# Optimization experiments

Hardware: AMD Instinct MI355X
Metric: run time of the kernel (lower is better)

## Reference

```python
import math
import jax, jax.numpy as jnp
import numpy as np

D_K = 1024


def setup_inputs() -> dict:
    key = jax.random.key(0)
    ks = jax.random.split(key, 7)
    B, L, d_model, d_k = 8, 2048, 1024, D_K
    source = jax.random.normal(ks[0], (B, L, d_model), dtype=jnp.float32)
    # torch nn.Linear params: weight (out, in), bias (out,)
    Wq = jax.random.normal(ks[1], (d_k, d_model), dtype=jnp.float32) * 0.02
    Wk = jax.random.normal(ks[2], (d_k, d_model), dtype=jnp.float32) * 0.02
    Wv = jax.random.normal(ks[3], (d_k, d_model), dtype=jnp.float32) * 0.02
    bq = jnp.zeros((d_k,), dtype=jnp.float32)
    bk = jnp.zeros((d_k,), dtype=jnp.float32)
    bv = jnp.zeros((d_k,), dtype=jnp.float32)
    return {"source": source, "Wq": Wq, "bq": bq, "Wk": Wk, "bk": bk,
            "Wv": Wv, "bv": bv, "mask": 1}


def reference(source, Wq, bq, Wk, bk, Wv, bv, mask):
    # q,k,v: (B, L, d_k); torch Linear => x @ W.T + b
    q = jnp.einsum("bld,kd->blk", source, Wq) + bq
    k = jnp.einsum("bld,kd->blk", source, Wk) + bk
    v = jnp.einsum("bld,kd->blk", source, Wv) + bv  # target defaults to source
    L = source.shape[1]
    scores = jnp.einsum("blk,bmk->blm", q, k) / math.sqrt(D_K)  # (B, L, L)
    if mask:
        # -inf strictly above the diagonal (j > i)
        causal = jnp.triu(jnp.full((L, L), -jnp.inf, dtype=scores.dtype), k=1)
        scores = scores + causal
    # Faithful to original: Softmax(dim=1) -> normalize over axis 1 (rows)
    attention = jax.nn.softmax(scores, axis=1)
    output = jnp.einsum("blm,bmk->blk", attention, v)  # (B, L, d_k)
    return (output, attention)
```

## Files before the change

kernel.cpp:

```cpp
#include <hip/hip_runtime.h>
#include <hip/hip_bf16.h>

typedef __attribute__((ext_vector_type(8))) __bf16 bf16x8;
typedef __attribute__((ext_vector_type(8))) unsigned short us8;
typedef __attribute__((ext_vector_type(4))) float f32x4;
typedef long long ll;

#define GLD(gp, lp) __builtin_amdgcn_global_load_lds( \
    (const __attribute__((address_space(1))) void*)(gp), \
    (__attribute__((address_space(3))) void*)(lp), 16, 0, 0)

#define SBAR()  asm volatile("s_barrier" ::: "memory")
#define VMCNT4  asm volatile("s_waitcnt vmcnt(4)" ::: "memory")
#define VMCNT0  asm volatile("s_waitcnt vmcnt(0)" ::: "memory")
#define SCHED0() __builtin_amdgcn_sched_barrier(0)

template<int OP>
__global__ __launch_bounds__(512) void gemm8(
    const __bf16* __restrict__ A, const __bf16* __restrict__ B,
    void* __restrict__ Cp, const float* __restrict__ bias,
    const int* __restrict__ maskp, float* __restrict__ part,
    int K, int lda, int ldb, int ldc,
    ll batchA, ll batchB, ll batchC)
{
    __shared__ __bf16 LA[2][256][64];
    __shared__ __bf16 LB[2][256][64];

    const int bx = blockIdx.x, by = blockIdx.y, bz = blockIdx.z;
    const int t    = threadIdx.x;
    const int w    = t >> 6, lane = t & 63;
    const int wrm  = w >> 2, wcn  = w & 3;
    const int fr   = lane & 15, fq = lane >> 4;
    const int row0 = bx * 256;
    const int col0 = by * 256;
    const int msk  = (OP >= 1) ? maskp[0] : 0;

    if (OP == 1 && msk && by > bx) {
        __bf16* C = (__bf16*)Cp + (ll)bz * batchC;
        bf16x8 z = {};
        #pragma unroll 4
        for (int pass = 0; pass < 16; ++pass) {
            int r = pass * 16 + (t >> 5);
            *(bf16x8*)&C[(ll)(row0 + r) * ldc + col0 + (t & 31) * 8] = z;
        }
        if (part && t < 256) part[((ll)bx * 8 + bz) * 2048 + col0 + t] = 0.f;
        return;
    }

    int NT = K / 64;
    if (OP == 2 && msk) NT = (row0 + 256) / 64;
    const int NI = NT / 2;

    const __bf16* Ab = A + (ll)bz * batchA;
    const __bf16* Bb = B + (ll)bz * batchB;

    const int srow = lane >> 3;
    const int cg   = (lane & 7) ^ srow;

    auto stageA = [&](int kt, int h, int slot) {
        #pragma unroll
        for (int is = 0; is < 2; ++is)
            GLD(Ab + (ll)(row0 + h*128 + is*64 + w*8 + srow) * lda + kt*64 + cg*8,
                &LA[slot][h*128 + is*64 + w*8][0]);
    };
    auto stageB = [&](int kt, int h, int slot) {
        #pragma unroll
        for (int is = 0; is < 2; ++is)
            GLD(Bb + (ll)(col0 + h*128 + is*64 + w*8 + srow) * ldb + kt*64 + cg*8,
                &LB[slot][h*128 + is*64 + w*8][0]);
    };
    auto rdA = [&](int slot, int row, int g) -> bf16x8 {
        return *(const bf16x8*)&LA[slot][row][(g ^ (row & 7)) << 3];
    };
    auto rdB = [&](int slot, int row, int g) -> bf16x8 {
        return *(const bf16x8*)&LB[slot][row][(g ^ (row & 7)) << 3];
    };

    f32x4  acc[8][4] = {};
    bf16x8 bB[4][2];

    stageA(0, 0, 0); stageA(0, 1, 0);
    stageB(0, 0, 0); stageB(0, 1, 0);
    stageB(1, 0, 1); stageB(1, 1, 1);
    VMCNT4;
    SBAR();

#define PHASE(SLOT, Q, STG, VMC) \
  { \
    if (Q == 0) { \
      _Pragma("unroll") for (int j = 0; j < 4; ++j) \
      _Pragma("unroll") for (int ks = 0; ks < 2; ++ks) \
        bB[j][ks] = rdB(SLOT, wcn*64 + j*16 + fr, ks*4 + fq); \
    } \
    bf16x8 bA[2][2]; \
    _Pragma("unroll") for (int fi = 0; fi < 2; ++fi) \
    _Pragma("unroll") for (int ks = 0; ks < 2; ++ks) \
      bA[fi][ks] = rdA(SLOT, wrm*128 + (Q*2+fi)*16 + fr, ks*4 + fq); \
    STG; \
    VMC; \
    SBAR(); SCHED0(); \
    __builtin_amdgcn_s_setprio(1); \
    _Pragma("unroll") for (int fi = 0; fi < 2; ++fi) \
    _Pragma("unroll") for (int j = 0; j < 4; ++j) \
    _Pragma("unroll") for (int ks = 0; ks < 2; ++ks) \
      acc[Q*2+fi][j] = __builtin_amdgcn_mfma_f32_16x16x32_bf16( \
          bA[fi][ks], bB[j][ks], acc[Q*2+fi][j], 0, 0, 0); \
    __builtin_amdgcn_s_setprio(0); \
    SCHED0(); SBAR(); \
  }

    for (int i = 0; i < NI; ++i) {
        const bool nl = (i < NI - 1);
        const int k1 = 2*i + 1, k2 = 2*i + 2, k3 = 2*i + 3;
        PHASE(0, 0, stageA(k1, 0, 1), );
        PHASE(0, 1, stageA(k1, 1, 1), );
        PHASE(0, 2, if (nl) stageB(k2, 0, 0), );
        PHASE(0, 3, if (nl) stageB(k2, 1, 0), if (nl) { VMCNT4; } else { VMCNT0; });
        PHASE(1, 0, if (nl) stageA(k2, 0, 0), );
        PHASE(1, 1, if (nl) stageA(k2, 1, 0), );
        PHASE(1, 2, if (nl) stageB(k3, 0, 1), );
        PHASE(1, 3, if (nl) stageB(k3, 1, 1), if (nl) { VMCNT4; });
    }
#undef PHASE

    const ll coff = (ll)bz * batchC;
    float s4[4] = {0.f, 0.f, 0.f, 0.f};
    #pragma unroll
    for (int fi = 0; fi < 8; ++fi)
    #pragma unroll
    for (int j = 0; j < 4; ++j)
    #pragma unroll
    for (int r4 = 0; r4 < 4; ++r4) {
        const int row = row0 + wrm*128 + fi*16 + fq*4 + r4;
        const int col = col0 + wcn*64 + j*16 + fr;
        float v = acc[fi][j][r4];
        if (OP == 0) {
            v += bias[col];
            ((__bf16*)Cp)[coff + (ll)row * ldc + col] = (__bf16)v;
        } else if (OP == 1) {
            float e = (msk && col > row) ? 0.f : __expf(v * 0.03125f);
            __bf16 eb = (__bf16)e;
            ((__bf16*)Cp)[coff + (ll)row * ldc + col] = eb;
            s4[j] += (float)eb;
        } else {
            ((float*)Cp)[coff + (ll)row * ldc + col] = v;
        }
    }
    if (OP == 1 && part != nullptr) {
        float* red = (float*)&LA[0][0][0];
        __syncthreads();
        #pragma unroll
        for (int j = 0; j < 4; ++j)
            red[(wrm*4 + fq)*256 + wcn*64 + j*16 + fr] = s4[j];
        __syncthreads();
        if (t < 256) {
            float tot = 0.f;
            #pragma unroll
            for (int r = 0; r < 8; ++r) tot += red[r*256 + t];
            part[((ll)bx * 8 + bz) * 2048 + col0 + t] = tot;
        }
    }
}

__global__ __launch_bounds__(512) void pv64(
    const __bf16* __restrict__ E, const __bf16* __restrict__ VT,
    const float* __restrict__ inv, float* __restrict__ out,
    float* __restrict__ attn, const int* __restrict__ maskp)
{
    __shared__ __bf16 LA[2][64][64];
    __shared__ __bf16 LB[2][256][64];

    const int bxr = (int)gridDim.x - 1 - (int)blockIdx.x;
    const int by = blockIdx.y, bz = blockIdx.z;
    const int t = threadIdx.x, w = t >> 6, lane = t & 63;
    const int wrm = w >> 2, wcn = w & 3;
    const int fr = lane & 15, fq = lane >> 4;
    const int row0 = bxr * 64, col0 = by * 256;
    const int msk = maskp[0];

    int NT = msk ? ((bxr + 2) & ~1) : 32;
    const int NI = NT / 2;

    const __bf16* Ab = E  + (ll)bz * 2048 * 2048;
    const __bf16* Bb = VT + (ll)bz * 1024 * 2048;

    const int srow = lane >> 3;
    const int cg   = (lane & 7) ^ srow;

    auto stageA = [&](int kt, int slot) {
        GLD(Ab + (ll)(row0 + w*8 + srow) * 2048 + kt*64 + cg*8,
            &LA[slot][w*8][0]);
    };
    auto stageB = [&](int kt, int slot) {
        #pragma unroll
        for (int h = 0; h < 2; ++h)
        #pragma unroll
        for (int is = 0; is < 2; ++is)
            GLD(Bb + (ll)(col0 + h*128 + is*64 + w*8 + srow) * 2048 + kt*64 + cg*8,
                &LB[slot][h*128 + is*64 + w*8][0]);
    };
    auto rdA = [&](int slot, int row, int g) -> bf16x8 {
        return *(const bf16x8*)&LA[slot][row][(g ^ (row & 7)) << 3];
    };
    auto rdB = [&](int slot, int row, int g) -> bf16x8 {
        return *(const bf16x8*)&LB[slot][row][(g ^ (row & 7)) << 3];
    };

    f32x4  acc[2][4] = {};
    bf16x8 bB[4][2];

    stageA(0, 0); stageB(0, 0);
    stageB(1, 1);
    VMCNT4;
    SBAR();

#define PHASEP(SLOT, Q, STG, VMC) \
  { \
    if (Q == 0) { \
      _Pragma("unroll") for (int j = 0; j < 4; ++j) \
      _Pragma("unroll") for (int ks = 0; ks < 2; ++ks) \
        bB[j][ks] = rdB(SLOT, wcn*64 + j*16 + fr, ks*4 + fq); \
    } \
    bf16x8 bA[2]; \
    _Pragma("unroll") for (int ks = 0; ks < 2; ++ks) \
      bA[ks] = rdA(SLOT, wrm*32 + Q*16 + fr, ks*4 + fq); \
    STG; \
    VMC; \
    SBAR(); SCHED0(); \
    __builtin_amdgcn_s_setprio(1); \
    _Pragma("unroll") for (int j = 0; j < 4; ++j) \
    _Pragma("unroll") for (int ks = 0; ks < 2; ++ks) \
      acc[Q][j] = __builtin_amdgcn_mfma_f32_16x16x32_bf16( \
          bA[ks], bB[j][ks], acc[Q][j], 0, 0, 0); \
    __builtin_amdgcn_s_setprio(0); \
    SCHED0(); SBAR(); \
  }

    for (int i = 0; i < NI; ++i) {
        const bool nl = (i < NI - 1);
        const int kb = 2*i + 1, ka2 = 2*i + 2, kb2 = 2*i + 3;
        PHASEP(0, 0, stageA(kb, 1), );
        PHASEP(0, 1, if (nl) stageB(ka2, 0),
                     if (nl) { VMCNT4; } else { VMCNT0; });
        PHASEP(1, 0, if (nl) stageA(ka2, 0), );
        PHASEP(1, 1, if (nl) stageB(kb2, 1),
                     if (nl) { VMCNT4; });
    }
#undef PHASEP

    #pragma unroll
    for (int qf = 0; qf < 2; ++qf)
    #pragma unroll
    for (int j = 0; j < 4; ++j)
    #pragma unroll
    for (int r4 = 0; r4 < 4; ++r4) {
        const int row = row0 + wrm*32 + qf*16 + fq*4 + r4;
        const int col = col0 + wcn*64 + j*16 + fr;
        out[(ll)bz*2048*1024 + (ll)row*1024 + col] = acc[qf][j][r4];
    }

    {
        const int c0 = by * 512;
        const int ct = (t & 63) * 8;
        float iv[8];
        #pragma unroll
        for (int e = 0; e < 8; ++e) iv[e] = inv[bz*2048 + c0 + ct + e];
        const int r00 = t >> 6;
        #pragma unroll 2
        for (int ri = 0; ri < 8; ++ri) {
            const int row = row0 + ri*8 + r00;
            bf16x8 ev = *(const bf16x8*)&Ab[(ll)row*2048 + c0 + ct];
            f32x4 lo, hi;
            #pragma unroll
            for (int e = 0; e < 4; ++e) {
                lo[e] = (float)ev[e]     * iv[e];
                hi[e] = (float)ev[e + 4] * iv[e + 4];
            }
            float* ao = attn + (ll)bz*2048*2048 + (ll)row*2048 + c0 + ct;
            ((f32x4*)ao)[0] = lo;
            ((f32x4*)ao)[1] = hi;
        }
    }
}

__global__ __launch_bounds__(256) void cvt_k(const float* __restrict__ in,
                                             __bf16* __restrict__ out, int n8)
{
    const int i = blockIdx.x * 256 + threadIdx.x;
    if (i >= n8) return;
    const f32x4* p = (const f32x4*)(in + (ll)i * 8);
    f32x4 a = p[0], b = p[1];
    bf16x8 h;
    #pragma unroll
    for (int j = 0; j < 4; ++j) { h[j] = (__bf16)a[j]; h[j + 4] = (__bf16)b[j]; }
    *(bf16x8*)(out + (ll)i * 8) = h;
}

__global__ __launch_bounds__(256) void cvtb_k(const float* __restrict__ q,
                                              const float* __restrict__ k,
                                              const float* __restrict__ v,
                                              float* __restrict__ bb)
{
    const int i = blockIdx.x * 256 + threadIdx.x;
    bb[i] = (i < 1024) ? q[i] : (i < 2048) ? k[i - 1024] : v[i - 2048];
}

__global__ __launch_bounds__(256) void rsum_k(const float* __restrict__ part,
                                              float* __restrict__ inv)
{
    const int idx = blockIdx.x * 256 + threadIdx.x;
    const int b = idx >> 11, m = idx & 2047;
    float s = 0.f;
    #pragma unroll
    for (int lc = 0; lc < 8; ++lc) s += part[((ll)lc * 8 + b) * 2048 + m];
    inv[idx] = 1.0f / s;
}

__global__ __launch_bounds__(256) void vtp_k(const __bf16* __restrict__ qkv,
                                             const float* __restrict__ inv,
                                             __bf16* __restrict__ vt)
{
    __shared__ __bf16 tile[64][72];
    const int t  = threadIdx.x;
    const int m0 = blockIdx.x * 64;
    const int k0 = blockIdx.y * 64;
    const int b  = blockIdx.z;

    const __bf16* V = qkv + (ll)b * 2048 * 3072 + 2048;
    #pragma unroll
    for (int h = 0; h < 2; ++h) {
        int r = (t >> 3) + h * 32;
        int c = (t & 7) * 8;
        int m = m0 + r;
        const float iv = inv[b * 2048 + m];
        bf16x8 v = *(const bf16x8*)&V[(ll)m * 3072 + k0 + c];
        bf16x8 o;
        #pragma unroll
        for (int j = 0; j < 8; ++j) o[j] = (__bf16)((float)v[j] * iv);
        *(bf16x8*)&tile[r][c] = o;
    }
    __syncthreads();
    __bf16* O = vt + (ll)b * 1024 * 2048;
    #pragma unroll
    for (int h = 0; h < 2; ++h) {
        int k = (t >> 3) + h * 32;
        int m = (t & 7) * 8;
        bf16x8 o;
        #pragma unroll
        for (int j = 0; j < 8; ++j) o[j] = tile[m + j][k];
        *(bf16x8*)&O[(ll)(k0 + k) * 2048 + m0 + m] = o;
    }
}

__global__ __launch_bounds__(256) void vt_k(const unsigned short* __restrict__ qkv,
                                            unsigned short* __restrict__ vt)
{
    __shared__ unsigned short tile[64][72];
    const int t  = threadIdx.x;
    const int m0 = blockIdx.x * 64;
    const int k0 = blockIdx.y * 64;
    const int b  = blockIdx.z;

    const unsigned short* V = qkv + (ll)b * 2048 * 3072 + 2048;
    #pragma unroll
    for (int h = 0; h < 2; ++h) {
        int r = (t >> 3) + h * 32;
        int c = (t & 7) * 8;
        us8 v = *(const us8*)&V[(ll)(m0 + r) * 3072 + k0 + c];
        *(us8*)&tile[r][c] = v;
    }
    __syncthreads();
    unsigned short* O = vt + (ll)b * 1024 * 2048;
    #pragma unroll
    for (int h = 0; h < 2; ++h) {
        int k = (t >> 3) + h * 32;
        int m = (t & 7) * 8;
        us8 o;
        #pragma unroll
        for (int j = 0; j < 8; ++j) o[j] = tile[m + j][k];
        *(us8*)&O[(ll)(k0 + k) * 2048 + m0 + m] = o;
    }
}

__global__ __launch_bounds__(256) void colsum_k(const __bf16* __restrict__ E,
                                                float* __restrict__ part)
{
    const int lc = blockIdx.x, mc = blockIdx.y, b = blockIdx.z;
    const int m  = mc * 256 + threadIdx.x;
    const __bf16* p = E + (ll)b * 2048 * 2048 + (ll)(lc * 256) * 2048 + m;
    float s = 0.f;
    #pragma unroll 4
    for (int l = 0; l < 256; ++l) s += (float)p[(ll)l * 2048];
    part[((ll)lc * 8 + b) * 2048 + m] = s;
}

__global__ __launch_bounds__(256) void norm_k(const __bf16* __restrict__ E,
                                              const float* __restrict__ part,
                                              float* __restrict__ attn,
                                              __bf16* __restrict__ attn_bf)
{
    const int lc = blockIdx.x, mc = blockIdx.y, b = blockIdx.z;
    const int m  = mc * 256 + threadIdx.x;
    float s = 0.f;
    #pragma unroll
    for (int j = 0; j < 8; ++j) s += part[((ll)j * 8 + b) * 2048 + m];
    const float iv = 1.0f / s;
    const __bf16* p = E + (ll)b * 2048 * 2048 + (ll)(lc * 256) * 2048 + m;
    float*  qo = attn    + (ll)b * 2048 * 2048 + (ll)(lc * 256) * 2048 + m;
    __bf16* ro = attn_bf + (ll)b * 2048 * 2048 + (ll)(lc * 256) * 2048 + m;
    #pragma unroll 4
    for (int l = 0; l < 256; ++l) {
        float a = (float)p[(ll)l * 2048] * iv;
        qo[(ll)l * 2048] = a;
        ro[(ll)l * 2048] = (__bf16)a;
    }
}

extern "C" void kernel_launch(void* const* d_in, const int* in_sizes, int n_in,
                              void* d_out, int out_size, void* d_ws, size_t ws_size,
                              hipStream_t stream)
{
    const float* X   = (const float*)d_in[0];
    const float* Wq  = (const float*)d_in[1];
    const float* bq  = (const float*)d_in[2];
    const float* Wk  = (const float*)d_in[3];
    const float* bk  = (const float*)d_in[4];
    const float* Wv  = (const float*)d_in[5];
    const float* bv  = (const float*)d_in[6];
    const int*   msk = (const int*)d_in[7];

    float* out  = (float*)d_out;
    float* attn = out + (ll)8 * 2048 * 1024;

    __bf16* Xb = (__bf16*)attn;
    __bf16* Wb = Xb + (ll)16384 * 1024;
    float*  bb = (float*)(Wb + (ll)3072 * 1024);

    __bf16* qkv = (__bf16*)d_ws;
    __bf16* vt  = qkv + (ll)16384 * 3072;

    cvt_k<<<dim3(8192), 256, 0, stream>>>(X, Xb, 16384 * 1024 / 8);
    cvt_k<<<dim3(512),  256, 0, stream>>>(Wq, Wb,               1024 * 1024 / 8);
    cvt_k<<<dim3(512),  256, 0, stream>>>(Wk, Wb + 1024 * 1024, 1024 * 1024 / 8);
    cvt_k<<<dim3(512),  256, 0, stream>>>(Wv, Wb + 2048 * 1024, 1024 * 1024 / 8);
    cvtb_k<<<dim3(12),  256, 0, stream>>>(bq, bk, bv, bb);

    gemm8<0><<<dim3(64, 12, 1), 512, 0, stream>>>(
        Xb, Wb, qkv, bb, msk, nullptr,
        1024, 1024, 1024, 3072, 0LL, 0LL, 0LL);

    const size_t need_fused =
        (size_t)(16384ll*3072 + 8ll*1024*2048 + 8ll*2048*2048) * 2
        + (size_t)(8*8*2048 + 8*2048) * 4;

    if (ws_size >= need_fused) {
        __bf16* E   = vt + (ll)8 * 1024 * 2048;
        float*  prt = (float*)(E + (ll)8 * 2048 * 2048);
        float*  inv = prt + 8 * 8 * 2048;

        gemm8<1><<<dim3(8, 8, 8), 512, 0, stream>>>(
            qkv, qkv + 1024, E, nullptr, msk, prt,
            1024, 3072, 3072, 2048,
            (ll)2048 * 3072, (ll)2048 * 3072, (ll)2048 * 2048);

        rsum_k<<<dim3(64), 256, 0, stream>>>(prt, inv);

        vtp_k<<<dim3(32, 16, 8), 256, 0, stream>>>(qkv, inv, vt);

        pv64<<<dim3(32, 4, 8), 512, 0, stream>>>(E, vt, inv, out, attn, msk);
    } else {
        __bf16* E   = (__bf16*)d_out;
        float*  prt = (float*)(vt + (ll)8 * 1024 * 2048);
        __bf16* attn_bf = qkv;

        vt_k<<<dim3(32, 16, 8), 256, 0, stream>>>((const unsigned short*)qkv,
                                                  (unsigned short*)vt);

        gemm8<1><<<dim3(8, 8, 8), 512, 0, stream>>>(
            qkv, qkv + 1024, E, nullptr, msk, nullptr,
            1024, 3072, 3072, 2048,
            (ll)2048 * 3072, (ll)2048 * 3072, (ll)2048 * 2048);

        colsum_k<<<dim3(8, 8, 8), 256, 0, stream>>>(E, prt);
        norm_k<<<dim3(8, 8, 8), 256, 0, stream>>>(E, prt, attn, attn_bf);

        gemm8<2><<<dim3(8, 4, 8), 512, 0, stream>>>(
            attn_bf, vt, out, nullptr, msk, nullptr,
            2048, 2048, 2048, 1024,
            (ll)2048 * 2048, (ll)1024 * 2048, (ll)2048 * 1024);
    }
}
```

Before: 336.7 us.

## Split attention normalization out of PV kernel and reorder PV block mapping

Moves the attention-probability write (E scaled by column inverse sums, widened to fp32) out of the PV GEMM epilogue into a separate norm2m_k kernel. That kernel zero-fills the masked upper tiles directly without reading E. The PV grid is flattened so the four column blocks of a row tile run next to each other, aiming for better reuse of the E row tile in cache. The cost is an extra launch and a separate pass over E, and the new kernel uses 4-byte per-thread strided row accesses that may coalesce less well than the old 8-wide vector stores.

```diff
diff --git a/kernel.cpp b/kernel.cpp
--- a/kernel.cpp
+++ b/kernel.cpp
@@ -164,14 +164,15 @@
 
 __global__ __launch_bounds__(512) void pv64(
     const __bf16* __restrict__ E, const __bf16* __restrict__ VT,
-    const float* __restrict__ inv, float* __restrict__ out,
-    float* __restrict__ attn, const int* __restrict__ maskp)
+    float* __restrict__ out, const int* __restrict__ maskp)
 {
     __shared__ __bf16 LA[2][64][64];
     __shared__ __bf16 LB[2][256][64];
 
-    const int bxr = (int)gridDim.x - 1 - (int)blockIdx.x;
-    const int by = blockIdx.y, bz = blockIdx.z;
+    const int n   = blockIdx.x;
+    const int by  = n & 3;
+    const int bxr = 31 - (n >> 2);
+    const int bz  = blockIdx.z;
     const int t = threadIdx.x, w = t >> 6, lane = t & 63;
     const int wrm = w >> 2, wcn = w & 3;
     const int fr = lane & 15, fq = lane >> 4;
@@ -258,29 +259,28 @@
         const int col = col0 + wcn*64 + j*16 + fr;
         out[(ll)bz*2048*1024 + (ll)row*1024 + col] = acc[qf][j][r4];
     }
-
-    {
-        const int c0 = by * 512;
-        const int ct = (t & 63) * 8;
-        float iv[8];
-        #pragma unroll
-        for (int e = 0; e < 8; ++e) iv[e] = inv[bz*2048 + c0 + ct + e];
-        const int r00 = t >> 6;
-        #pragma unroll 2
-        for (int ri = 0; ri < 8; ++ri) {
-            const int row = row0 + ri*8 + r00;
-            bf16x8 ev = *(const bf16x8*)&Ab[(ll)row*2048 + c0 + ct];
-            f32x4 lo, hi;
-            #pragma unroll
-            for (int e = 0; e < 4; ++e) {
-                lo[e] = (float)ev[e]     * iv[e];
-                hi[e] = (float)ev[e + 4] * iv[e + 4];
-            }
-            float* ao = attn + (ll)bz*2048*2048 + (ll)row*2048 + c0 + ct;
-            ((f32x4*)ao)[0] = lo;
-            ((f32x4*)ao)[1] = hi;
-        }
-    }
+}
+
+__global__ __launch_bounds__(256) void norm2m_k(const __bf16* __restrict__ E,
+                                                const float* __restrict__ inv,
+                                                float* __restrict__ attn,
+                                                const int* __restrict__ maskp)
+{
+    const int lc = blockIdx.x, mc = blockIdx.y, b = blockIdx.z;
+    const int m  = mc * 256 + threadIdx.x;
+    float* qo = attn + (ll)b * 2048 * 2048 + (ll)(lc * 256) * 2048 + m;
+
+    if (maskp[0] && mc > lc) {
+        #pragma unroll 4
+        for (int l = 0; l < 256; ++l)
+            qo[(ll)l * 2048] = 0.f;
+        return;
+    }
+    const float iv = inv[b * 2048 + m];
+    const __bf16* p = E + (ll)b * 2048 * 2048 + (ll)(lc * 256) * 2048 + m;
+    #pragma unroll 4
+    for (int l = 0; l < 256; ++l)
+        qo[(ll)l * 2048] = (float)p[(ll)l * 2048] * iv;
 }
 
 __global__ __launch_bounds__(256) void cvt_k(const float* __restrict__ in,
@@ -467,7 +467,9 @@
 
         vtp_k<<<dim3(32, 16, 8), 256, 0, stream>>>(qkv, inv, vt);
 
-        pv64<<<dim3(32, 4, 8), 512, 0, stream>>>(E, vt, inv, out, attn, msk);
+        norm2m_k<<<dim3(8, 8, 8), 256, 0, stream>>>(E, inv, attn, msk);
+
+        pv64<<<dim3(128, 1, 8), 512, 0, stream>>>(E, vt, out, msk);
     } else {
         __bf16* E   = (__bf16*)d_out;
         float*  prt = (float*)(vt + (ll)8 * 1024 * 2048);
```

Measured after the change: 343.3 us. About the same (+2.0%).
